# Kernel optimization log

Measured on AMD Instinct MI355X. Metric: run time of the kernel, lower is better.

## Reference

```python
import jax, jax.numpy as jnp
import numpy as np

N, D, K = 8192, 2048, 256
# amnesic weights at train iteration 0: _i = 2 < n1 = 20 -> l = 0
W1 = 0.5  # (_i - 1 - l) / _i
W2 = 0.5  # (1 + l) / _i


def setup_inputs() -> dict:
    key = jax.random.key(0)
    k1, k2 = jax.random.split(key)
    x = jax.random.normal(k1, (N, D), dtype=jnp.float32)
    V0 = 0.1 * jax.random.normal(k2, (D, K), dtype=jnp.float32)  # init eigen vectors
    return {"x": x, "V0": V0}


def reference(x, V0):
    # x: [N, D] input batch; V0: [D, K] unnormalized eigenvector estimates (_v)
    d0 = jnp.linalg.norm(V0, axis=0)  # per-column norms, as in init_eigen_vectors setter

    def step(r, inp):
        v, d = inp  # v: [D] current unnormalized component, d: scalar norm
        # CCIPCA update: v' = w1*v + w2 * r^T (r v) / d
        u = W1 * v + (W2 / d) * (r.T @ (r @ v))
        dn = jnp.linalg.norm(u)
        vn = u / dn
        # deflate residual: r <- r - (r vn) vn^T
        r = r - jnp.outer(r @ vn, vn)
        return r, vn

    _, vns = jax.lax.scan(step, x, (V0.T, d0))  # vns: [K, D] normalized components
    # project original input on updated components: x.mm(self.v)
    return x @ vns.T  # [N, K]
```

## Files before the change

kernel.cpp:

```cpp
#include <hip/hip_runtime.h>
#include <math.h>

#define NN 8192
#define DD 2048
#define KK 256
#define NB 256
#define RPB 8
#define NGRP 16
#define GSZ 16

__device__ __forceinline__ float blockReduceSum(float val, float* sdata) {
    for (int off = 32; off > 0; off >>= 1)
        val += __shfl_down(val, off, 64);
    int wid = threadIdx.x >> 6;
    int lane = threadIdx.x & 63;
    __syncthreads();
    if (lane == 0) sdata[wid] = val;
    __syncthreads();
    return sdata[0] + sdata[1] + sdata[2] + sdata[3];
}

__device__ __forceinline__ float agload(const float* p) {
    return __hip_atomic_load(p, __ATOMIC_RELAXED, __HIP_MEMORY_SCOPE_AGENT);
}
__device__ __forceinline__ void agstore(float* p, float v) {
    __hip_atomic_store(p, v, __ATOMIC_RELAXED, __HIP_MEMORY_SCOPE_AGENT);
}

__device__ __forceinline__ void gbar2(unsigned* bar, int b, unsigned* gen_local) {
    __syncthreads();
    if (threadIdx.x == 0) {
        unsigned g0 = *gen_local;
        int grp = b >> 4;
        unsigned* gcnt = bar + (size_t)grp * 64;
        unsigned* ggen = bar + 1024 + (size_t)grp * 64;
        unsigned* rcnt = bar + 2048;
        unsigned* rgen = bar + 2112;
        unsigned prev = __hip_atomic_fetch_add(gcnt, 1u, __ATOMIC_RELAXED, __HIP_MEMORY_SCOPE_AGENT);
        if (prev == GSZ - 1u) {
            unsigned prevr = __hip_atomic_fetch_add(rcnt, 1u, __ATOMIC_RELAXED, __HIP_MEMORY_SCOPE_AGENT);
            if (prevr == NGRP - 1u) {
                __hip_atomic_store(rcnt, 0u, __ATOMIC_RELAXED, __HIP_MEMORY_SCOPE_AGENT);
                asm volatile("s_waitcnt vmcnt(0)" ::: "memory");
                __hip_atomic_store(rgen, g0 + 1u, __ATOMIC_RELAXED, __HIP_MEMORY_SCOPE_AGENT);
            } else {
                while (__hip_atomic_load(rgen, __ATOMIC_RELAXED, __HIP_MEMORY_SCOPE_AGENT) == g0)
                    __builtin_amdgcn_s_sleep(1);
            }
            __hip_atomic_store(gcnt, 0u, __ATOMIC_RELAXED, __HIP_MEMORY_SCOPE_AGENT);
            asm volatile("s_waitcnt vmcnt(0)" ::: "memory");
            __hip_atomic_store(ggen, g0 + 1u, __ATOMIC_RELAXED, __HIP_MEMORY_SCOPE_AGENT);
        } else {
            while (__hip_atomic_load(ggen, __ATOMIC_RELAXED, __HIP_MEMORY_SCOPE_AGENT) == g0)
                __builtin_amdgcn_s_sleep(1);
        }
    }
    *gen_local += 1u;
    __syncthreads();
}

__global__ void ktranspose(const float* __restrict__ V0, float* __restrict__ V0T) {
    __shared__ float tile[32][33];
    int bx = blockIdx.x;
    int by = blockIdx.y;
    int tx = threadIdx.x % 32;
    int ty = threadIdx.x / 32;
    for (int r = ty; r < 32; r += 8)
        tile[r][tx] = V0[(size_t)(bx * 32 + r) * KK + by * 32 + tx];
    __syncthreads();
    for (int r = ty; r < 32; r += 8)
        V0T[(size_t)(by * 32 + r) * DD + bx * 32 + tx] = tile[tx][r];
}

__global__ void kd0(const float* __restrict__ V0T, float* __restrict__ d0) {
    __shared__ float sdata[4];
    int k = blockIdx.x;
    float acc = 0.f;
    for (int j = threadIdx.x; j < DD; j += 256) {
        float v = V0T[(size_t)k * DD + j];
        acc += v * v;
    }
    float s = blockReduceSum(acc, sdata);
    if (threadIdx.x == 0) d0[k] = sqrtf(s);
}

__global__ void ksyrk(const float* __restrict__ x, float* __restrict__ G) {
    __shared__ float As[32][68];
    __shared__ float Bs[32][68];
    int t = blockIdx.x;
    int bj = (int)((sqrtf(8.0f * (float)t + 1.0f) - 1.0f) * 0.5f);
    while ((bj + 1) * (bj + 2) / 2 <= t) ++bj;
    while (bj * (bj + 1) / 2 > t) --bj;
    int bi = t - bj * (bj + 1) / 2;
    int a0 = bi * 64, b0 = bj * 64;
    int tid = threadIdx.x;
    int al = tid % 64;
    int nl0 = tid / 64;
    int tr = tid / 16, tc = tid % 16;
    float acc[4][4] = {};
    for (int n0 = 0; n0 < NN; n0 += 32) {
        for (int pass = 0; pass < 8; ++pass) {
            int nl = nl0 + pass * 4;
            As[nl][al] = x[(size_t)(n0 + nl) * DD + a0 + al];
            Bs[nl][al] = x[(size_t)(n0 + nl) * DD + b0 + al];
        }
        __syncthreads();
        for (int kk2 = 0; kk2 < 32; ++kk2) {
            float4 a4 = *(const float4*)&As[kk2][tr * 4];
            float4 b4 = *(const float4*)&Bs[kk2][tc * 4];
            float a[4] = {a4.x, a4.y, a4.z, a4.w};
            float b[4] = {b4.x, b4.y, b4.z, b4.w};
            for (int i = 0; i < 4; ++i)
                for (int j = 0; j < 4; ++j)
                    acc[i][j] += a[i] * b[j];
        }
        __syncthreads();
    }
    for (int i = 0; i < 4; ++i) {
        float4 o = make_float4(acc[i][0], acc[i][1], acc[i][2], acc[i][3]);
        *(float4*)&G[(size_t)(a0 + tr * 4 + i) * DD + b0 + tc * 4] = o;
    }
    if (bi != bj) {
        for (int i = 0; i < 4; ++i)
            for (int j = 0; j < 4; ++j)
                G[(size_t)(b0 + tc * 4 + j) * DD + a0 + tr * 4 + i] = acc[i][j];
    }
}

__global__ void kmatvecG(const float* __restrict__ G, const float* __restrict__ v,
                         float* __restrict__ s) {
    __shared__ float vs[DD];
    int tid = threadIdx.x;
    for (int t2 = 0; t2 < 8; ++t2) vs[tid + t2 * 256] = v[tid + t2 * 256];
    __syncthreads();
    int wave = tid >> 6, lane = tid & 63;
    int row = blockIdx.x * 4 + wave;
    const float* Gr = G + (size_t)row * DD;
    float a = 0.f;
    for (int c = 0; c < 8; ++c) {
        int idx = lane * 4 + c * 256;
        float4 gq = *(const float4*)(Gr + idx);
        float4 vq = *(const float4*)(vs + idx);
        a += gq.x * vq.x + gq.y * vq.y + gq.z * vq.z + gq.w * vq.w;
    }
    for (int off = 32; off > 0; off >>= 1) a += __shfl_down(a, off, 64);
    if (lane == 0) s[row] = a;
}

__global__ void kstep1(const float* __restrict__ G, const float* __restrict__ V0T,
                       const float* __restrict__ d0, const float* __restrict__ s,
                       float* __restrict__ g, float* __restrict__ Vn, int k) {
    __shared__ float u[DD];
    __shared__ float sdata[4];
    __shared__ float sinv;
    int tid = threadIdx.x;
    const float* v = V0T + (size_t)k * DD;
    float cf = 0.5f / d0[k];
    float acc = 0.f;
    for (int t2 = 0; t2 < 8; ++t2) {
        int j = tid + t2 * 256;
        float uj = 0.5f * v[j] + cf * s[j];
        u[j] = uj;
        acc += uj * uj;
    }
    float n2 = blockReduceSum(acc, sdata);
    if (tid == 0) sinv = 1.0f / sqrtf(n2);
    __syncthreads();
    float inv = sinv;
    if (blockIdx.x == 0) {
        for (int t2 = 0; t2 < 8; ++t2) {
            int j = tid + t2 * 256;
            Vn[(size_t)k * DD + j] = u[j] * inv;
        }
    }
    int wave = tid >> 6, lane = tid & 63;
    int row = blockIdx.x * 4 + wave;
    const float* Gr = G + (size_t)row * DD;
    float a = 0.f;
    for (int c = 0; c < 8; ++c) {
        int idx = lane * 4 + c * 256;
        float4 gq = *(const float4*)(Gr + idx);
        float4 uq = *(const float4*)(u + idx);
        a += gq.x * uq.x + gq.y * uq.y + gq.z * uq.z + gq.w * uq.w;
    }
    for (int off = 32; off > 0; off >>= 1) a += __shfl_down(a, off, 64);
    if (lane == 0) g[row] = a * inv;
}

__global__ void kstep2(float* __restrict__ G, const float* __restrict__ V0T,
                       const float* __restrict__ Vn, const float* __restrict__ g,
                       float* __restrict__ s_next, int k, int knext) {
    __shared__ float vn_s[DD];
    __shared__ float h_s[DD];
    __shared__ float w_s[DD];
    __shared__ float sdata[4];
    int tid = threadIdx.x;
    float acc = 0.f;
    for (int t2 = 0; t2 < 8; ++t2) {
        int j = tid + t2 * 256;
        float vnj = Vn[(size_t)k * DD + j];
        float gj = g[j];
        vn_s[j] = vnj;
        h_s[j] = gj;
        w_s[j] = V0T[(size_t)knext * DD + j];
        acc += vnj * gj;
    }
    float c = blockReduceSum(acc, sdata);
    for (int t2 = 0; t2 < 8; ++t2) {
        int j = tid + t2 * 256;
        h_s[j] -= c * vn_s[j];
    }
    __syncthreads();
    int wave = tid >> 6, lane = tid & 63;
    int row = blockIdx.x * 4 + wave;
    float vni = vn_s[row], gi = g[row];
    float* Gr = G + (size_t)row * DD;
    float a = 0.f;
    for (int cc = 0; cc < 8; ++cc) {
        int idx = lane * 4 + cc * 256;
        float4 Gq = *(float4*)(Gr + idx);
        float4 hq = *(const float4*)(h_s + idx);
        float4 vq = *(const float4*)(vn_s + idx);
        float4 wq = *(const float4*)(w_s + idx);
        Gq.x = Gq.x - vni * hq.x - gi * vq.x;
        Gq.y = Gq.y - vni * hq.y - gi * vq.y;
        Gq.z = Gq.z - vni * hq.z - gi * vq.z;
        Gq.w = Gq.w - vni * hq.w - gi * vq.w;
        a += Gq.x * wq.x + Gq.y * wq.y + Gq.z * wq.z + Gq.w * wq.w;
        *(float4*)(Gr + idx) = Gq;
    }
    for (int off = 32; off > 0; off >>= 1) a += __shfl_down(a, off, 64);
    if (lane == 0) s_next[row] = a;
}

__global__ void __launch_bounds__(1024, 4) kloop4(
    float* __restrict__ G, const float* __restrict__ V0T,
    const float* __restrict__ d0v, float* __restrict__ Vn,
    float* __restrict__ gbuf, float* __restrict__ wbuf,
    float* __restrict__ acc, unsigned* bar) {
    __shared__ float vbuf[2][DD];
    __shared__ float gs[DD];
    __shared__ float vx[DD];
    __shared__ float partg[16], partw[16];

    const int tid = threadIdx.x;
    const int b = blockIdx.x;
    const int wave = tid >> 6, lane = tid & 63;
    const int rowi = wave >> 1;
    const int half = wave & 1;
    const int row = b * RPB + rowi;
    const int d0i = tid, d1i = tid + 1024;
    const int ib = half * 1024 + lane * 4;
    const float* Gr = G + (size_t)row * DD;
    unsigned gen = 0;

    float4 Gq[4];
    #pragma unroll
    for (int c = 0; c < 4; ++c) Gq[c] = *(const float4*)(Gr + ib + c * 256);

    vbuf[0][d0i] = 0.f;
    vbuf[0][d1i] = 0.f;
    vx[d0i] = V0T[d0i];
    vx[d1i] = V0T[d1i];
    __syncthreads();
    {
        float aw = 0.f;
        #pragma unroll
        for (int c = 0; c < 4; ++c) {
            float4 xq = *(const float4*)(vx + ib + c * 256);
            aw += Gq[c].x * xq.x + Gq[c].y * xq.y + Gq[c].z * xq.z + Gq[c].w * xq.w;
        }
        for (int off = 32; off > 0; off >>= 1) aw += __shfl_down(aw, off, 64);
        if (lane == 0) partw[wave] = aw;
    }
    __syncthreads();
    if (tid < RPB) {
        int rg = b * RPB + tid;
        agstore(&wbuf[rg], partw[2 * tid] + partw[2 * tid + 1]);
    }
    if (tid == 0) {
        float a4 = 0.f, a7 = 0.f;
        for (int r = 0; r < RPB; ++r) {
            float wr = partw[2 * r] + partw[2 * r + 1];
            a4 += wr * wr;
            a7 += wr * vx[b * RPB + r];
        }
        atomicAdd(&acc[3], a4);
        atomicAdd(&acc[6], a7);
    }
    gbar2(bar, b, &gen);

    for (int k = 0; k < KK; ++k) {
        const int p = k & 1;
        const float* vnp = vbuf[p];
        float* vnew = vbuf[p ^ 1];
        const float* gsrc = gbuf + (size_t)p * DD;
        const float* wsrc = wbuf + (size_t)p * DD;
        float* gdst = gbuf + (size_t)(p ^ 1) * DD;
        float* wdst = wbuf + (size_t)(p ^ 1) * DD;
        const float* vk = V0T + (size_t)k * DD;
        const float* as = acc + (size_t)k * 8;

        float A1 = agload(&as[0]), A2 = agload(&as[1]), A3 = agload(&as[2]);
        float A4 = agload(&as[3]), A5 = agload(&as[4]), A6 = agload(&as[5]);
        float A7 = agload(&as[6]), A8 = agload(&as[7]);
        float d0k = d0v[k];
        float cf = 0.5f / d0k;
        float c_s = A1;
        float alpha = A2 - A1 * A3;
        float beta = A3;
        float ss = A4 + alpha * alpha + beta * beta * A8
                 - 2.f * alpha * A6 - 2.f * beta * A5 + 2.f * alpha * beta * A1;
        float vks = A7 - alpha * A3 - beta * A2;
        float n2 = 0.25f * d0k * d0k + cf * vks + cf * cf * ss;
        float inv = 1.0f / sqrtf(n2);

        float g0 = agload(&gsrc[d0i]), g1 = agload(&gsrc[d1i]);
        float w0 = agload(&wsrc[d0i]), w1 = agload(&wsrc[d1i]);
        float vk0 = vk[d0i], vk1 = vk[d1i];
        float vp0 = vnp[d0i], vp1 = vnp[d1i];
        gs[d0i] = g0;
        gs[d1i] = g1;
        float u0 = 0.5f * vk0 + cf * (w0 - alpha * vp0 - beta * g0);
        float u1 = 0.5f * vk1 + cf * (w1 - alpha * vp1 - beta * g1);
        vnew[d0i] = u0 * inv;
        vnew[d1i] = u1 * inv;
        if (k < KK - 1) {
            vx[d0i] = V0T[(size_t)(k + 1) * DD + d0i];
            vx[d1i] = V0T[(size_t)(k + 1) * DD + d1i];
        }
        __syncthreads();

        if (tid < RPB) {
            int rg = b * RPB + tid;
            agstore(&Vn[(size_t)k * DD + rg], vnew[rg]);
        }
        if (k == KK - 1) break;

        {
            float a_r = vnp[row];
            float g_r = gs[row];
            float b_r = g_r - c_s * a_r;
            float ag = 0.f, aw = 0.f;
            #pragma unroll
            for (int c = 0; c < 4; ++c) {
                int idx = ib + c * 256;
                float4 gq = *(const float4*)(gs + idx);
                float4 vq = *(const float4*)(vnp + idx);
                float4 nq = *(const float4*)(vnew + idx);
                float4 xq = *(const float4*)(vx + idx);
                Gq[c].x -= a_r * gq.x + b_r * vq.x;
                Gq[c].y -= a_r * gq.y + b_r * vq.y;
                Gq[c].z -= a_r * gq.z + b_r * vq.z;
                Gq[c].w -= a_r * gq.w + b_r * vq.w;
                ag += Gq[c].x * nq.x + Gq[c].y * nq.y + Gq[c].z * nq.z + Gq[c].w * nq.w;
                aw += Gq[c].x * xq.x + Gq[c].y * xq.y + Gq[c].z * xq.z + Gq[c].w * xq.w;
            }
            for (int off = 32; off > 0; off >>= 1) {
                ag += __shfl_down(ag, off, 64);
                aw += __shfl_down(aw, off, 64);
            }
            if (lane == 0) { partg[wave] = ag; partw[wave] = aw; }
        }
        __syncthreads();
        if (tid < RPB) {
            int rg = b * RPB + tid;
            agstore(&gdst[rg], partg[2 * tid] + partg[2 * tid + 1]);
            agstore(&wdst[rg], partw[2 * tid] + partw[2 * tid + 1]);
        }
        if (tid < 8) {
            float sacc = 0.f;
            for (int r = 0; r < RPB; ++r) {
                int rg = b * RPB + r;
                float gr = partg[2 * r] + partg[2 * r + 1];
                float wr = partw[2 * r] + partw[2 * r + 1];
                float vnr = vnew[rg];
                float vxr = vx[rg];
                float t;
                switch (tid) {
                    case 0: t = vnr * gr; break;
                    case 1: t = gr * vxr; break;
                    case 2: t = vnr * vxr; break;
                    case 3: t = wr * wr; break;
                    case 4: t = wr * gr; break;
                    case 5: t = wr * vnr; break;
                    case 6: t = wr * vxr; break;
                    default: t = gr * gr; break;
                }
                sacc += t;
            }
            atomicAdd(&acc[(size_t)(k + 1) * 8 + tid], sacc);
        }
        gbar2(bar, b, &gen);
    }
}

__global__ void kout(const float* __restrict__ x, const float* __restrict__ Vn,
                     float* __restrict__ out) {
    __shared__ float As[32][68];
    __shared__ float Bs[32][68];
    int i0 = blockIdx.x * 64;
    int k0 = blockIdx.y * 64;
    int tid = threadIdx.x;
    int tr = tid / 16;
    int tc = tid % 16;
    float acc[4][4] = {};
    for (int j0 = 0; j0 < DD; j0 += 32) {
        int c = tid % 32;
        int r0 = tid / 32;
        for (int pass = 0; pass < 8; ++pass) {
            int rr = r0 + pass * 8;
            As[c][rr] = x[(size_t)(i0 + rr) * DD + j0 + c];
            Bs[c][rr] = Vn[(size_t)(k0 + rr) * DD + j0 + c];
        }
        __syncthreads();
        for (int kk = 0; kk < 32; ++kk) {
            float4 a4 = *(const float4*)&As[kk][tr * 4];
            float4 b4 = *(const float4*)&Bs[kk][tc * 4];
            float a[4] = {a4.x, a4.y, a4.z, a4.w};
            float b[4] = {b4.x, b4.y, b4.z, b4.w};
            for (int ar = 0; ar < 4; ++ar)
                for (int bc = 0; bc < 4; ++bc)
                    acc[ar][bc] += a[ar] * b[bc];
        }
        __syncthreads();
    }
    for (int ar = 0; ar < 4; ++ar) {
        float4 o = make_float4(acc[ar][0], acc[ar][1], acc[ar][2], acc[ar][3]);
        *(float4*)&out[(size_t)(i0 + tr * 4 + ar) * KK + k0 + tc * 4] = o;
    }
}

extern "C" void kernel_launch(void* const* d_in, const int* in_sizes, int n_in,
                              void* d_out, int out_size, void* d_ws, size_t ws_size,
                              hipStream_t stream) {
    const float* x  = (const float*)d_in[0];
    const float* V0 = (const float*)d_in[1];
    float* out = (float*)d_out;

    float* G    = (float*)d_ws;
    float* V0T  = G + (size_t)DD * DD;
    float* Vn   = V0T + (size_t)KK * DD;
    float* gbuf = Vn + (size_t)KK * DD;
    float* wbuf = gbuf + 2 * DD;
    float* d0   = wbuf + 2 * DD;
    float* acc  = d0 + KK;
    unsigned* bar = (unsigned*)(acc + (size_t)KK * 8);

    ktranspose<<<dim3(DD / 32, KK / 32), 256, 0, stream>>>(V0, V0T);
    kd0<<<KK, 256, 0, stream>>>(V0T, d0);
    ksyrk<<<528, 256, 0, stream>>>(x, G);

    hipMemsetAsync(bar, 0, 2176 * sizeof(unsigned), stream);
    hipMemsetAsync(gbuf, 0, DD * sizeof(float), stream);
    hipMemsetAsync(acc, 0, (size_t)KK * 8 * sizeof(float), stream);

    void* kargs[] = {(void*)&G, (void*)&V0T, (void*)&d0, (void*)&Vn,
                     (void*)&gbuf, (void*)&wbuf, (void*)&acc, (void*)&bar};
    hipError_t cerr = hipLaunchCooperativeKernel(kloop4, dim3(NB), dim3(1024),
                                                 kargs, 0, stream);
    if (cerr != hipSuccess) {
        float* g = gbuf;
        float* sbuf = wbuf;
        kmatvecG<<<512, 256, 0, stream>>>(G, V0T, sbuf);
        for (int k = 0; k < KK; ++k) {
            float* s_cur = sbuf + (k & 1) * DD;
            float* s_nxt = sbuf + ((k + 1) & 1) * DD;
            kstep1<<<512, 256, 0, stream>>>(G, V0T, d0, s_cur, g, Vn, k);
            if (k < KK - 1)
                kstep2<<<512, 256, 0, stream>>>(G, V0T, Vn, g, s_nxt, k, k + 1);
        }
    }

    kout<<<dim3(NN / 64, KK / 64), 256, 0, stream>>>(x, Vn, out);
}
```

Before: 3.471 ms.

## Replace generation barrier with per-step monotonic counters and per-block scalar partials

The two-level generation-based grid barrier, which had to reset its counters each time, is replaced by one counter set per iteration slot: group counters feed a root counter, and every block spins until the root reaches the group count, with no reset or release store. The eight per-step scalar atomicAdds into a shared accumulator become plain stores of per-block partials into a [K][8][NB] buffer, which each block reduces with wavefronts at the start of the next step. The reduction loads are also issued alongside the g/w/vk loads before a block sync. The aim is to cut barrier latency and atomic contention on the critical serial loop, at the cost of a larger workspace and a 256-element reduction per step.

Result: faster. 3.270 ms (-5.8%).

```diff
diff --git a/kernel.cpp b/kernel.cpp
--- a/kernel.cpp
+++ b/kernel.cpp
@@ -27,35 +27,18 @@
     __hip_atomic_store(p, v, __ATOMIC_RELAXED, __HIP_MEMORY_SCOPE_AGENT);
 }
 
-__device__ __forceinline__ void gbar2(unsigned* bar, int b, unsigned* gen_local) {
-    __syncthreads();
+__device__ __forceinline__ void dfsync(unsigned* grpc, unsigned* rootc, int slot, int b) {
     if (threadIdx.x == 0) {
-        unsigned g0 = *gen_local;
+        asm volatile("s_waitcnt vmcnt(0)" ::: "memory");
         int grp = b >> 4;
-        unsigned* gcnt = bar + (size_t)grp * 64;
-        unsigned* ggen = bar + 1024 + (size_t)grp * 64;
-        unsigned* rcnt = bar + 2048;
-        unsigned* rgen = bar + 2112;
-        unsigned prev = __hip_atomic_fetch_add(gcnt, 1u, __ATOMIC_RELAXED, __HIP_MEMORY_SCOPE_AGENT);
-        if (prev == GSZ - 1u) {
-            unsigned prevr = __hip_atomic_fetch_add(rcnt, 1u, __ATOMIC_RELAXED, __HIP_MEMORY_SCOPE_AGENT);
-            if (prevr == NGRP - 1u) {
-                __hip_atomic_store(rcnt, 0u, __ATOMIC_RELAXED, __HIP_MEMORY_SCOPE_AGENT);
-                asm volatile("s_waitcnt vmcnt(0)" ::: "memory");
-                __hip_atomic_store(rgen, g0 + 1u, __ATOMIC_RELAXED, __HIP_MEMORY_SCOPE_AGENT);
-            } else {
-                while (__hip_atomic_load(rgen, __ATOMIC_RELAXED, __HIP_MEMORY_SCOPE_AGENT) == g0)
-                    __builtin_amdgcn_s_sleep(1);
-            }
-            __hip_atomic_store(gcnt, 0u, __ATOMIC_RELAXED, __HIP_MEMORY_SCOPE_AGENT);
-            asm volatile("s_waitcnt vmcnt(0)" ::: "memory");
-            __hip_atomic_store(ggen, g0 + 1u, __ATOMIC_RELAXED, __HIP_MEMORY_SCOPE_AGENT);
-        } else {
-            while (__hip_atomic_load(ggen, __ATOMIC_RELAXED, __HIP_MEMORY_SCOPE_AGENT) == g0)
-                __builtin_amdgcn_s_sleep(1);
-        }
-    }
-    *gen_local += 1u;
+        unsigned* gw = grpc + ((size_t)slot * NGRP + grp) * 16;
+        unsigned* rw = rootc + (size_t)slot * 16;
+        unsigned prev = __hip_atomic_fetch_add(gw, 1u, __ATOMIC_RELAXED, __HIP_MEMORY_SCOPE_AGENT);
+        if (prev == GSZ - 1u)
+            __hip_atomic_fetch_add(rw, 1u, __ATOMIC_RELAXED, __HIP_MEMORY_SCOPE_AGENT);
+        while (__hip_atomic_load(rw, __ATOMIC_RELAXED, __HIP_MEMORY_SCOPE_AGENT) < (unsigned)NGRP)
+            __builtin_amdgcn_s_sleep(2);
+    }
     __syncthreads();
 }
 
@@ -233,14 +216,15 @@
     if (lane == 0) s_next[row] = a;
 }
 
-__global__ void __launch_bounds__(1024, 4) kloop4(
+__global__ void __launch_bounds__(1024, 4) kloop5(
     float* __restrict__ G, const float* __restrict__ V0T,
     const float* __restrict__ d0v, float* __restrict__ Vn,
     float* __restrict__ gbuf, float* __restrict__ wbuf,
-    float* __restrict__ acc, unsigned* bar) {
+    float* __restrict__ accbuf, unsigned* rootc, unsigned* grpc) {
     __shared__ float vbuf[2][DD];
     __shared__ float gs[DD];
     __shared__ float vx[DD];
+    __shared__ float scal[8];
     __shared__ float partg[16], partw[16];
 
     const int tid = threadIdx.x;
@@ -252,7 +236,6 @@
     const int d0i = tid, d1i = tid + 1024;
     const int ib = half * 1024 + lane * 4;
     const float* Gr = G + (size_t)row * DD;
-    unsigned gen = 0;
 
     float4 Gq[4];
     #pragma unroll
@@ -278,17 +261,17 @@
         int rg = b * RPB + tid;
         agstore(&wbuf[rg], partw[2 * tid] + partw[2 * tid + 1]);
     }
-    if (tid == 0) {
-        float a4 = 0.f, a7 = 0.f;
+    if (tid < 8) {
+        float sacc = 0.f;
         for (int r = 0; r < RPB; ++r) {
+            int rg = b * RPB + r;
             float wr = partw[2 * r] + partw[2 * r + 1];
-            a4 += wr * wr;
-            a7 += wr * vx[b * RPB + r];
-        }
-        atomicAdd(&acc[3], a4);
-        atomicAdd(&acc[6], a7);
-    }
-    gbar2(bar, b, &gen);
+            if (tid == 3) sacc += wr * wr;
+            else if (tid == 6) sacc += wr * vx[rg];
+        }
+        agstore(&accbuf[(size_t)tid * NB + b], sacc);
+    }
+    dfsync(grpc, rootc, 0, b);
 
     for (int k = 0; k < KK; ++k) {
         const int p = k & 1;
@@ -299,11 +282,21 @@
         float* gdst = gbuf + (size_t)(p ^ 1) * DD;
         float* wdst = wbuf + (size_t)(p ^ 1) * DD;
         const float* vk = V0T + (size_t)k * DD;
-        const float* as = acc + (size_t)k * 8;
-
-        float A1 = agload(&as[0]), A2 = agload(&as[1]), A3 = agload(&as[2]);
-        float A4 = agload(&as[3]), A5 = agload(&as[4]), A6 = agload(&as[5]);
-        float A7 = agload(&as[6]), A8 = agload(&as[7]);
+
+        if (wave < 8) {
+            const float* ap = accbuf + (size_t)k * (8 * NB) + (size_t)wave * NB + lane * 4;
+            float sp = agload(ap) + agload(ap + 1) + agload(ap + 2) + agload(ap + 3);
+            for (int off = 32; off > 0; off >>= 1) sp += __shfl_down(sp, off, 64);
+            if (lane == 0) scal[wave] = sp;
+        }
+        float g0 = agload(&gsrc[d0i]), g1 = agload(&gsrc[d1i]);
+        float w0 = agload(&wsrc[d0i]), w1 = agload(&wsrc[d1i]);
+        float vk0 = vk[d0i], vk1 = vk[d1i];
+        float vp0 = vnp[d0i], vp1 = vnp[d1i];
+        __syncthreads();
+
+        float A1 = scal[0], A2 = scal[1], A3 = scal[2], A4 = scal[3];
+        float A5 = scal[4], A6 = scal[5], A7 = scal[6], A8 = scal[7];
         float d0k = d0v[k];
         float cf = 0.5f / d0k;
         float c_s = A1;
@@ -315,10 +308,6 @@
         float n2 = 0.25f * d0k * d0k + cf * vks + cf * cf * ss;
         float inv = 1.0f / sqrtf(n2);
 
-        float g0 = agload(&gsrc[d0i]), g1 = agload(&gsrc[d1i]);
-        float w0 = agload(&wsrc[d0i]), w1 = agload(&wsrc[d1i]);
-        float vk0 = vk[d0i], vk1 = vk[d1i];
-        float vp0 = vnp[d0i], vp1 = vnp[d1i];
         gs[d0i] = g0;
         gs[d1i] = g1;
         float u0 = 0.5f * vk0 + cf * (w0 - alpha * vp0 - beta * g0);
@@ -389,9 +378,9 @@
                 }
                 sacc += t;
             }
-            atomicAdd(&acc[(size_t)(k + 1) * 8 + tid], sacc);
-        }
-        gbar2(bar, b, &gen);
+            agstore(&accbuf[(size_t)(k + 1) * (8 * NB) + (size_t)tid * NB + b], sacc);
+        }
+        dfsync(grpc, rootc, k + 1, b);
     }
 }
 
@@ -444,20 +433,21 @@
     float* gbuf = Vn + (size_t)KK * DD;
     float* wbuf = gbuf + 2 * DD;
     float* d0   = wbuf + 2 * DD;
-    float* acc  = d0 + KK;
-    unsigned* bar = (unsigned*)(acc + (size_t)KK * 8);
+    float* accbuf = d0 + KK;
+    unsigned* rootc = (unsigned*)(accbuf + (size_t)KK * 8 * NB);
+    unsigned* grpc  = rootc + (size_t)KK * 16;
 
     ktranspose<<<dim3(DD / 32, KK / 32), 256, 0, stream>>>(V0, V0T);
     kd0<<<KK, 256, 0, stream>>>(V0T, d0);
     ksyrk<<<528, 256, 0, stream>>>(x, G);
 
-    hipMemsetAsync(bar, 0, 2176 * sizeof(unsigned), stream);
+    hipMemsetAsync(rootc, 0, ((size_t)KK * 16 + (size_t)KK * NGRP * 16) * sizeof(unsigned), stream);
     hipMemsetAsync(gbuf, 0, DD * sizeof(float), stream);
-    hipMemsetAsync(acc, 0, (size_t)KK * 8 * sizeof(float), stream);
 
     void* kargs[] = {(void*)&G, (void*)&V0T, (void*)&d0, (void*)&Vn,
-                     (void*)&gbuf, (void*)&wbuf, (void*)&acc, (void*)&bar};
-    hipError_t cerr = hipLaunchCooperativeKernel(kloop4, dim3(NB), dim3(1024),
+                     (void*)&gbuf, (void*)&wbuf, (void*)&accbuf,
+                     (void*)&rootc, (void*)&grpc};
+    hipError_t cerr = hipLaunchCooperativeKernel(kloop5, dim3(NB), dim3(1024),
                                                  kargs, 0, stream);
     if (cerr != hipSuccess) {
         float* g = gbuf;
```
